# Kernel optimization log

Hardware: AMD Instinct MI355X
Metric: run time of the kernel (lower is better)

## Reference

```python
import jax, jax.numpy as jnp
import numpy as np

N, E, F_IN, HID, HEADS, NCLS = 50000, 800000, 512, 64, 4, 40
NEG_SLOPE = 0.2


def setup_inputs() -> dict:
    key = jax.random.key(0)
    ks = jax.random.split(key, 12)
    x = jax.random.normal(ks[0], (N, F_IN), jnp.float32)
    edge_index = jax.random.randint(ks[1], (2, E), 0, N, jnp.int32)
    edge_weight = jnp.ones((E,), jnp.float32)
    s1 = 1.0 / np.sqrt(F_IN)
    s2 = 1.0 / np.sqrt(HID * HEADS)
    return {
        "x": x,
        "edge_index": edge_index,
        "edge_weight": edge_weight,
        "W1": jax.random.normal(ks[2], (F_IN, HEADS * HID), jnp.float32) * s1,
        "a_src1": jax.random.normal(ks[3], (HEADS, HID), jnp.float32) * s1,
        "a_dst1": jax.random.normal(ks[4], (HEADS, HID), jnp.float32) * s1,
        "b1": jnp.zeros((HEADS * HID,), jnp.float32),
        "W2": jax.random.normal(ks[5], (HEADS * HID, NCLS), jnp.float32) * s2,
        "a_src2": jax.random.normal(ks[6], (1, NCLS), jnp.float32) * s2,
        "a_dst2": jax.random.normal(ks[7], (1, NCLS), jnp.float32) * s2,
        "b2": jnp.zeros((NCLS,), jnp.float32),
    }


def _gat_layer(x, src, dst, ew, W, a_s, a_d, b, heads, n):
    c = W.shape[1] // heads
    h = (x @ W).reshape(n, heads, c)                      # [N,H,C]
    alpha_s = jnp.einsum('nhc,hc->nh', h, a_s)            # [N,H]
    alpha_d = jnp.einsum('nhc,hc->nh', h, a_d)
    e = jax.nn.leaky_relu(alpha_s[src] + alpha_d[dst], NEG_SLOPE)  # [Et,H]
    # segment softmax over destination nodes (self-loops guarantee nonempty segs)
    m = jax.ops.segment_max(e, dst, num_segments=n)
    ex = jnp.exp(e - m[dst])
    denom = jax.ops.segment_sum(ex, dst, num_segments=n)
    alpha = ex / (denom[dst] + 1e-16)                     # [Et,H]
    alpha = alpha * ew[:, None]
    msg = h[src] * alpha[:, :, None]                      # [Et,H,C]
    out = jax.ops.segment_sum(msg, dst, num_segments=n)   # [N,H,C]
    return out.reshape(n, heads * c) + b


def reference(x, edge_index, edge_weight, W1, a_src1, a_dst1, b1, W2, a_src2, a_dst2, b2):
    n = x.shape[0]
    loop = jnp.arange(n, dtype=edge_index.dtype)
    src = jnp.concatenate([edge_index[0], loop])
    dst = jnp.concatenate([edge_index[1], loop])
    ew = jnp.concatenate([edge_weight, jnp.ones((n,), edge_weight.dtype)])
    h = _gat_layer(x, src, dst, ew, W1, a_src1, a_dst1, b1, HEADS, n)
    h = jax.nn.relu(h)  # dropout p=0.0, eval mode: no-op
    out = _gat_layer(h, src, dst, ew, W2, a_src2, a_dst2, b2, 1, n)
    return out  # Identity (log_softmax_return=False)
```

## Files before the change

kernel.cpp:

```cpp
#include <hip/hip_runtime.h>
#include <math.h>

#define N_NODES 50000
#define N_EDGES 800000
#define ET (N_EDGES + N_NODES)
#define F_IN 512
#define HID 64
#define HEADS 4
#define C1 (HEADS * HID)
#define NCLS 40
#define NEG_SLOPE 0.2f

#define BUK_SHIFT 7
#define BUK_NODES (1 << BUK_SHIFT)
#define NBUK ((N_NODES + BUK_NODES - 1) / BUK_NODES)
#define CAP 4096
#define NREP 4
#define SUBCAP (CAP / NREP)
#define BF_STRIDE 8
#define EPB_A 2048
#define NBLK_A ((ET + EPB_A - 1) / EPB_A)
#define NG1 ((N_NODES + 127) / 128)
#define RCAP 2560

typedef __attribute__((ext_vector_type(8))) short short8;
typedef __attribute__((ext_vector_type(4))) float floatx4;

__device__ __forceinline__ float leaky(float x) { return fmaxf(x, NEG_SLOPE * x); }

__device__ __forceinline__ unsigned short f2bf(float f) {
    unsigned u = __float_as_uint(f);
    u += 0x7fffu + ((u >> 16) & 1u);
    return (unsigned short)(u >> 16);
}
__device__ __forceinline__ float bf2f(unsigned short u) {
    return __uint_as_float(((unsigned)u) << 16);
}
__device__ __forceinline__ float bflo(unsigned v) { return __uint_as_float(v << 16); }
__device__ __forceinline__ float bfhi(unsigned v) { return __uint_as_float(v & 0xffff0000u); }

__device__ __forceinline__ void edge_sd(int e, const int* __restrict__ ei,
                                        const float* __restrict__ ew,
                                        int& s, int& d, float& w) {
    if (e < N_EDGES) { s = ei[e]; d = ei[N_EDGES + e]; w = ew[e]; }
    else             { s = d = e - N_EDGES; w = 1.f; }
}

__global__ void wt_prep_kernel(const float* __restrict__ W, unsigned short* __restrict__ WT,
                               int* __restrict__ bfill) {
    __shared__ float tile[32][33];
    int k0 = blockIdx.x * 32;
    int n0 = blockIdx.y * 32;
    int tx = threadIdx.x, ty = threadIdx.y;
    if (blockIdx.x == 0 && blockIdx.y == 0) {
        int tid = ty * 32 + tx;
        for (int i = tid; i < NBUK * NREP * BF_STRIDE; i += 256) bfill[i] = 0;
    }
    #pragma unroll
    for (int i = 0; i < 32; i += 8)
        tile[ty + i][tx] = W[(size_t)(k0 + ty + i) * C1 + n0 + tx];
    __syncthreads();
    #pragma unroll
    for (int i = 0; i < 32; i += 8)
        WT[(size_t)(n0 + ty + i) * F_IN + k0 + tx] = f2bf(tile[tx][ty + i]);
}

__global__ __launch_bounds__(512) void g1pa_kernel(const float* __restrict__ X,
                                                   const unsigned short* __restrict__ WT,
                                                   const float* __restrict__ a_s1,
                                                   const float* __restrict__ a_d1,
                                                   unsigned short* __restrict__ H,
                                                   float* __restrict__ AS,
                                                   float* __restrict__ AD,
                                                   const int* __restrict__ ei,
                                                   const float* __restrict__ ew,
                                                   int* __restrict__ bfill,
                                                   int2* __restrict__ SB) {
    __shared__ short As[128][40];
    __shared__ short Bs[256][40];
    __shared__ int lcnt[NBUK];
    __shared__ int lbase[NBUK];
    const int t = threadIdx.x;

    if (blockIdx.x >= NG1) {
        const int pb = blockIdx.x - NG1;
        const int rep = pb & (NREP - 1);
        const int e0 = pb * EPB_A + t;
        for (int i = t; i < NBUK; i += 512) lcnt[i] = 0;
        __syncthreads();
        int rx[4], ry[4];
        #pragma unroll
        for (int i = 0; i < 4; i++) {
            int e = e0 + i * 512;
            rx[i] = -1;
            ry[i] = 0;
            if (e < ET) {
                int s, d; float w;
                edge_sd(e, ei, ew, s, d, w);
                rx[i] = s | (d << 16);
                ry[i] = __float_as_int(w);
                atomicAdd(&lcnt[d >> BUK_SHIFT], 1);
            }
        }
        __syncthreads();
        for (int i = t; i < NBUK; i += 512) {
            int c = lcnt[i];
            lbase[i] = c ? atomicAdd(&bfill[(i * NREP + rep) * BF_STRIDE], c) : 0;
            lcnt[i] = 0;
        }
        __syncthreads();
        #pragma unroll
        for (int i = 0; i < 4; i++) {
            if (rx[i] != -1) {
                int b = ((unsigned)rx[i] >> 16) >> BUK_SHIFT;
                int r = atomicAdd(&lcnt[b], 1);
                int idx = lbase[b] + r;
                if (idx < SUBCAP)
                    SB[(size_t)b * CAP + rep * SUBCAP + idx] = make_int2(rx[i], ry[i]);
            }
        }
        return;
    }

    const int m0 = blockIdx.x * 128;
    const int lane = t & 63;
    const int wave = t >> 6;
    const int wm = wave >> 2;
    const int wn = wave & 3;
    const int l15 = lane & 15;
    const int quad = lane >> 4;

    const int ar = t >> 2;
    const int ac0 = (t & 3) * 8;
    const int gr = m0 + ar;
    const int bn = t >> 1;
    const int bc0 = (t & 1) * 16;

    floatx4 acc[4][4];
    #pragma unroll
    for (int i = 0; i < 4; i++)
        #pragma unroll
        for (int j = 0; j < 4; j++) acc[i][j] = (floatx4){0.f, 0.f, 0.f, 0.f};

    for (int k0 = 0; k0 < F_IN; k0 += 32) {
        float xv[8];
        if (gr < N_NODES) {
            const float4* p = (const float4*)(X + (size_t)gr * F_IN + k0 + ac0);
            float4 v0 = p[0], v1 = p[1];
            xv[0] = v0.x; xv[1] = v0.y; xv[2] = v0.z; xv[3] = v0.w;
            xv[4] = v1.x; xv[5] = v1.y; xv[6] = v1.z; xv[7] = v1.w;
        } else {
            #pragma unroll
            for (int i = 0; i < 8; i++) xv[i] = 0.f;
        }
        short8 av;
        #pragma unroll
        for (int i = 0; i < 8; i++) av[i] = (short)f2bf(xv[i]);
        *(short8*)&As[ar][ac0] = av;

        const short8* q = (const short8*)(WT + (size_t)bn * F_IN + k0 + bc0);
        *(short8*)&Bs[bn][bc0]     = q[0];
        *(short8*)&Bs[bn][bc0 + 8] = q[1];
        __syncthreads();

        short8 a[4], b[4];
        #pragma unroll
        for (int i = 0; i < 4; i++)
            a[i] = *(const short8*)&As[wm * 64 + i * 16 + l15][quad * 8];
        #pragma unroll
        for (int j = 0; j < 4; j++)
            b[j] = *(const short8*)&Bs[wn * 64 + j * 16 + l15][quad * 8];
        #pragma unroll
        for (int i = 0; i < 4; i++)
            #pragma unroll
            for (int j = 0; j < 4; j++)
                acc[i][j] = __builtin_amdgcn_mfma_f32_16x16x32_bf16(a[i], b[j], acc[i][j], 0, 0, 0);
        __syncthreads();
    }

    float asr[4], adr[4];
    #pragma unroll
    for (int j = 0; j < 4; j++) {
        asr[j] = a_s1[wn * HID + j * 16 + l15];
        adr[j] = a_d1[wn * HID + j * 16 + l15];
    }

    #pragma unroll
    for (int i = 0; i < 4; i++) {
        int rbase = m0 + wm * 64 + i * 16 + quad * 4;
        #pragma unroll
        for (int j = 0; j < 4; j++) {
            int col = wn * 64 + j * 16 + l15;
            #pragma unroll
            for (int r = 0; r < 4; r++) {
                int row = rbase + r;
                if (row < N_NODES) H[(size_t)row * C1 + col] = f2bf(acc[i][j][r]);
            }
        }
        #pragma unroll
        for (int r = 0; r < 4; r++) {
            int row = rbase + r;
            float s_ = acc[i][0][r] * asr[0] + acc[i][1][r] * asr[1]
                     + acc[i][2][r] * asr[2] + acc[i][3][r] * asr[3];
            float d_ = acc[i][0][r] * adr[0] + acc[i][1][r] * adr[1]
                     + acc[i][2][r] * adr[2] + acc[i][3][r] * adr[3];
            #pragma unroll
            for (int m = 8; m; m >>= 1) { s_ += __shfl_xor(s_, m); d_ += __shfl_xor(d_, m); }
            if (l15 == 0 && row < N_NODES) {
                AS[row * 4 + wn] = s_;
                AD[row * 4 + wn] = d_;
            }
        }
    }
}

__global__ __launch_bounds__(512) void place_kernel(const int* __restrict__ bfill,
                                                    const int2* __restrict__ SB,
                                                    int* __restrict__ row_ptr,
                                                    int2* __restrict__ E2) {
    __shared__ int2 rec[RCAP];
    __shared__ int lh[BUK_NODES];
    __shared__ int excl[BUK_NODES];
    __shared__ int psum[512];
    const int b = blockIdx.x;
    const int n0 = b << BUK_SHIFT;
    const int t = threadIdx.x;

    int v = 0;
    if (t < b) {
        #pragma unroll
        for (int r = 0; r < NREP; r++) {
            int c = bfill[(t * NREP + r) * BF_STRIDE];
            v += (c > SUBCAP) ? SUBCAP : c;
        }
    }
    psum[t] = v;
    __syncthreads();
    for (int s = 256; s > 0; s >>= 1) {
        if (t < s) psum[t] += psum[t + s];
        __syncthreads();
    }
    const int base_b = psum[0];

    int c[NREP], off[NREP];
    int tot = 0;
    #pragma unroll
    for (int r = 0; r < NREP; r++) {
        int cc = bfill[(b * NREP + r) * BF_STRIDE];
        c[r] = (cc > SUBCAP) ? SUBCAP : cc;
        off[r] = tot;
        tot += c[r];
    }
    if (t < BUK_NODES) lh[t] = 0;
    __syncthreads();
    #pragma unroll
    for (int r = 0; r < NREP; r++) {
        const int2* base = SB + (size_t)b * CAP + r * SUBCAP;
        for (int i = t; i < c[r]; i += 512) {
            int idx = off[r] + i;
            if (idx < RCAP) rec[idx] = base[i];
        }
    }
    if (tot > RCAP) tot = RCAP;
    __syncthreads();
    for (int i = t; i < tot; i += 512)
        atomicAdd(&lh[(((unsigned)rec[i].x) >> 16) - n0], 1);
    __syncthreads();
    if (t < BUK_NODES) excl[t] = lh[t];
    __syncthreads();
    #pragma unroll
    for (int s = 1; s < BUK_NODES; s <<= 1) {
        int u = (t < BUK_NODES && t >= s) ? excl[t - s] : 0;
        __syncthreads();
        if (t < BUK_NODES) excl[t] += u;
        __syncthreads();
    }
    if (t < BUK_NODES) {
        int e = excl[t] - lh[t];
        int node = n0 + t;
        if (node < N_NODES) row_ptr[node] = base_b + e;
        lh[t] = e;
    }
    __syncthreads();
    for (int i = t; i < tot; i += 512) {
        int2 v2 = rec[i];
        int d = (((unsigned)v2.x) >> 16) - n0;
        int pos = atomicAdd(&lh[d], 1);
        E2[base_b + pos] = make_int2(v2.x & 0xffff, v2.y);
    }
}

__global__ __launch_bounds__(256) void agg1_csr_kernel(const int* __restrict__ row_ptr,
                                                       const int2* __restrict__ E2,
                                                       const float* __restrict__ AS,
                                                       const float* __restrict__ AD,
                                                       const unsigned short* __restrict__ H,
                                                       const float* __restrict__ b1,
                                                       unsigned short* __restrict__ OUT) {
    int n = blockIdx.x * 4 + (threadIdx.x >> 6);
    int lane = threadIdx.x & 63;
    if (n >= N_NODES) return;
    int l15 = lane & 15;
    int h = lane >> 4;
    int c0 = lane * 4;
    int beg = row_ptr[n];
    int end = (n + 1 < N_NODES) ? row_ptr[n + 1] : ET;
    float ad = AD[n * 4 + h];
    float den = 0.f;
    float a0 = 0.f, a1 = 0.f, a2 = 0.f, a3 = 0.f;

    for (int base = beg; base < end; base += 16) {
        int m = end - base; if (m > 16) m = 16;
        float pw = 0.f; int s = 0;
        if (l15 < m) {
            int2 e = E2[base + l15];
            s = e.x;
            float pe = __expf(leaky(AS[e.x * 4 + h] + ad));
            den += pe;
            pw = pe * __int_as_float(e.y);
        }
        int p = 0;
        for (; p + 4 <= m; p += 4) {
            int s0 = __shfl(s, p);
            int s1 = __shfl(s, p + 1);
            int s2 = __shfl(s, p + 2);
            int s3 = __shfl(s, p + 3);
            uint2 u0 = *(const uint2*)(H + (size_t)s0 * C1 + c0);
            uint2 u1 = *(const uint2*)(H + (size_t)s1 * C1 + c0);
            uint2 u2 = *(const uint2*)(H + (size_t)s2 * C1 + c0);
            uint2 u3 = *(const uint2*)(H + (size_t)s3 * C1 + c0);
            float w0 = __shfl(pw, h * 16 + p);
            float w1 = __shfl(pw, h * 16 + p + 1);
            float w2 = __shfl(pw, h * 16 + p + 2);
            float w3 = __shfl(pw, h * 16 + p + 3);
            a0 += w0 * bflo(u0.x) + w1 * bflo(u1.x) + w2 * bflo(u2.x) + w3 * bflo(u3.x);
            a1 += w0 * bfhi(u0.x) + w1 * bfhi(u1.x) + w2 * bfhi(u2.x) + w3 * bfhi(u3.x);
            a2 += w0 * bflo(u0.y) + w1 * bflo(u1.y) + w2 * bflo(u2.y) + w3 * bflo(u3.y);
            a3 += w0 * bfhi(u0.y) + w1 * bfhi(u1.y) + w2 * bfhi(u2.y) + w3 * bfhi(u3.y);
        }
        for (; p < m; p++) {
            int s0 = __shfl(s, p);
            uint2 u0 = *(const uint2*)(H + (size_t)s0 * C1 + c0);
            float w0 = __shfl(pw, h * 16 + p);
            a0 += w0 * bflo(u0.x);
            a1 += w0 * bfhi(u0.x);
            a2 += w0 * bflo(u0.y);
            a3 += w0 * bfhi(u0.y);
        }
    }
    den += __shfl_xor(den, 1);
    den += __shfl_xor(den, 2);
    den += __shfl_xor(den, 4);
    den += __shfl_xor(den, 8);

    float r = 1.f / (den + 1e-16f);
    float4 bv = *(const float4*)(b1 + c0);
    float v0 = a0 * r + bv.x, v1 = a1 * r + bv.y, v2 = a2 * r + bv.z, v3 = a3 * r + bv.w;
    v0 = v0 > 0.f ? v0 : 0.f;
    v1 = v1 > 0.f ? v1 : 0.f;
    v2 = v2 > 0.f ? v2 : 0.f;
    v3 = v3 > 0.f ? v3 : 0.f;
    uint2 o;
    o.x = ((unsigned)f2bf(v1) << 16) | (unsigned)f2bf(v0);
    o.y = ((unsigned)f2bf(v3) << 16) | (unsigned)f2bf(v2);
    *(uint2*)(OUT + (size_t)n * C1 + c0) = o;
}

#define BROW 264
__global__ __launch_bounds__(512) void gemm2_mfma_kernel(const unsigned short* __restrict__ A,
                                                         const float* __restrict__ W2,
                                                         const float* __restrict__ a_s2,
                                                         const float* __restrict__ a_d2,
                                                         unsigned short* __restrict__ H2b,
                                                         float* __restrict__ AS2,
                                                         float* __restrict__ AD2) {
    __shared__ short As[256][40];
    __shared__ short Bs[48 * BROW];
    const int t = threadIdx.x;
    const int m0 = blockIdx.x * 256;
    const int lane = t & 63;
    const int wave = t >> 6;
    const int l15 = lane & 15;
    const int quad = lane >> 4;

    for (int i = t; i < 48 * 256; i += 512) {
        int n = i >> 8, k = i & 255;
        float v = (n < NCLS) ? W2[k * NCLS + n] : 0.f;
        Bs[n * BROW + k] = (short)f2bf(v);
    }

    const int ar = t >> 1;
    const int ac0 = (t & 1) * 16;

    floatx4 acc[2][3];
    #pragma unroll
    for (int i = 0; i < 2; i++)
        #pragma unroll
        for (int j = 0; j < 3; j++) acc[i][j] = (floatx4){0.f, 0.f, 0.f, 0.f};

    for (int k0 = 0; k0 < C1; k0 += 32) {
        const short8* q = (const short8*)(A + (size_t)(m0 + ar) * C1 + k0 + ac0);
        short8 v0 = q[0], v1 = q[1];
        __syncthreads();
        *(short8*)&As[ar][ac0]     = v0;
        *(short8*)&As[ar][ac0 + 8] = v1;
        __syncthreads();

        short8 a[2], b[3];
        #pragma unroll
        for (int i = 0; i < 2; i++)
            a[i] = *(const short8*)&As[wave * 32 + i * 16 + l15][quad * 8];
        #pragma unroll
        for (int j = 0; j < 3; j++)
            b[j] = *(const short8*)&Bs[(j * 16 + l15) * BROW + k0 + quad * 8];
        #pragma unroll
        for (int i = 0; i < 2; i++)
            #pragma unroll
            for (int j = 0; j < 3; j++)
                acc[i][j] = __builtin_amdgcn_mfma_f32_16x16x32_bf16(a[i], b[j], acc[i][j], 0, 0, 0);
    }

    float asr[3], adr[3];
    #pragma unroll
    for (int j = 0; j < 3; j++) {
        int col = j * 16 + l15;
        asr[j] = (col < NCLS) ? a_s2[col] : 0.f;
        adr[j] = (col < NCLS) ? a_d2[col] : 0.f;
    }

    #pragma unroll
    for (int i = 0; i < 2; i++) {
        #pragma unroll
        for (int r = 0; r < 4; r++) {
            int row = m0 + wave * 32 + i * 16 + quad * 4 + r;
            float s_ = acc[i][0][r] * asr[0] + acc[i][1][r] * asr[1] + acc[i][2][r] * asr[2];
            float d_ = acc[i][0][r] * adr[0] + acc[i][1][r] * adr[1] + acc[i][2][r] * adr[2];
            #pragma unroll
            for (int m = 8; m; m >>= 1) { s_ += __shfl_xor(s_, m); d_ += __shfl_xor(d_, m); }
            if (l15 == 0 && row < N_NODES) { AS2[row] = s_; AD2[row] = d_; }
            #pragma unroll
            for (int j = 0; j < 3; j++) {
                int col = j * 16 + l15;
                if (col < NCLS && row < N_NODES)
                    H2b[(size_t)row * NCLS + col] = f2bf(acc[i][j][r]);
            }
        }
    }
}

__global__ __launch_bounds__(256) void agg2_csr_kernel(const int* __restrict__ row_ptr,
                                                       const int2* __restrict__ E2,
                                                       const float* __restrict__ AS,
                                                       const float* __restrict__ AD,
                                                       const unsigned short* __restrict__ H2b,
                                                       const float* __restrict__ b2,
                                                       float* __restrict__ OUT) {
    int lane = threadIdx.x & 63;
    int n = blockIdx.x * 4 + (threadIdx.x >> 6);
    if (n >= N_NODES) return;
    int beg = row_ptr[n];
    int end = (n + 1 < N_NODES) ? row_ptr[n + 1] : ET;
    float ad = AD[n];
    bool act = lane < NCLS;
    float den = 0.f, acc = 0.f;

    for (int base = beg; base < end; base += 64) {
        int m = end - base; if (m > 64) m = 64;
        float pw = 0.f; int s = 0;
        if (lane < m) {
            int2 e = E2[base + lane];
            s = e.x;
            float pe = __expf(leaky(AS[e.x] + ad));
            den += pe;
            pw = pe * __int_as_float(e.y);
        }
        int p = 0;
        for (; p + 4 <= m; p += 4) {
            int s0 = __shfl(s, p);
            int s1 = __shfl(s, p + 1);
            int s2 = __shfl(s, p + 2);
            int s3 = __shfl(s, p + 3);
            float w0 = __shfl(pw, p);
            float w1 = __shfl(pw, p + 1);
            float w2 = __shfl(pw, p + 2);
            float w3 = __shfl(pw, p + 3);
            if (act) {
                float h0 = bf2f(H2b[(size_t)s0 * NCLS + lane]);
                float h1 = bf2f(H2b[(size_t)s1 * NCLS + lane]);
                float h2 = bf2f(H2b[(size_t)s2 * NCLS + lane]);
                float h3 = bf2f(H2b[(size_t)s3 * NCLS + lane]);
                acc += w0 * h0 + w1 * h1 + w2 * h2 + w3 * h3;
            }
        }
        for (; p < m; p++) {
            int s0 = __shfl(s, p);
            float w0 = __shfl(pw, p);
            if (act) acc += w0 * bf2f(H2b[(size_t)s0 * NCLS + lane]);
        }
    }
    den += __shfl_xor(den, 1);
    den += __shfl_xor(den, 2);
    den += __shfl_xor(den, 4);
    den += __shfl_xor(den, 8);
    den += __shfl_xor(den, 16);
    den += __shfl_xor(den, 32);
    if (act) {
        float r = 1.f / (den + 1e-16f);
        OUT[(size_t)n * NCLS + lane] = acc * r + b2[lane];
    }
}

extern "C" void kernel_launch(void* const* d_in, const int* in_sizes, int n_in,
                              void* d_out, int out_size, void* d_ws, size_t ws_size,
                              hipStream_t stream) {
    const float* x    = (const float*)d_in[0];
    const int*   ei   = (const int*)d_in[1];
    const float* ew   = (const float*)d_in[2];
    const float* W1   = (const float*)d_in[3];
    const float* a_s1 = (const float*)d_in[4];
    const float* a_d1 = (const float*)d_in[5];
    const float* b1   = (const float*)d_in[6];
    const float* W2   = (const float*)d_in[7];
    const float* a_s2 = (const float*)d_in[8];
    const float* a_d2 = (const float*)d_in[9];
    const float* b2   = (const float*)d_in[10];
    float* out = (float*)d_out;

    unsigned short* H1b  = (unsigned short*)d_ws;
    unsigned short* OUT1b = H1b + (size_t)N_NODES * C1;
    float* AS1  = (float*)(OUT1b + (size_t)N_NODES * C1);
    float* AD1  = AS1 + N_NODES * HEADS;
    int* row_ptr = (int*)(AD1 + N_NODES * HEADS);
    int* bfill = row_ptr + N_NODES;
    int2* E2  = (int2*)(bfill + NBUK * NREP * BF_STRIDE);
    unsigned short* WT = (unsigned short*)(E2 + ET);
    int2* SB = (int2*)(WT + (size_t)F_IN * C1);
    unsigned short* H2b = H1b;
    float* AS2  = (float*)(H2b + (size_t)N_NODES * NCLS);
    float* AD2  = AS2 + N_NODES;

    wt_prep_kernel<<<dim3(F_IN / 32, C1 / 32), dim3(32, 8), 0, stream>>>(W1, WT, bfill);

    g1pa_kernel<<<NG1 + NBLK_A, 512, 0, stream>>>(x, WT, a_s1, a_d1, H1b, AS1, AD1,
                                                  ei, ew, bfill, SB);

    place_kernel<<<NBUK, 512, 0, stream>>>(bfill, SB, row_ptr, E2);

    agg1_csr_kernel<<<(N_NODES + 3) / 4, 256, 0, stream>>>(row_ptr, E2, AS1, AD1, H1b, b1, OUT1b);

    gemm2_mfma_kernel<<<(N_NODES + 255) / 256, 512, 0, stream>>>(OUT1b, W2, a_s2, a_d2, H2b, AS2, AD2);
    agg2_csr_kernel<<<(N_NODES + 3) / 4, 256, 0, stream>>>(row_ptr, E2, AS2, AD2, H2b, b2, out);
}
```

Baseline: 317.4 us.

## Restructure gemm2 to smaller row tiles with whole-K A staging

The layer-2 GEMM now uses 64-row tiles with 256 threads, so 782 blocks are launched instead of 196 and the GPU's compute units are filled better. Each thread loads its full A row slice into registers up front, overlapping that load with the W2 conversion into shared memory, and then does a single sync. This removes the per-K-step double sync. It also adds a bounds guard on A rows. The trade-off is that each block re-converts the whole W2 into shared memory, so that setup work is repeated across four times as many blocks.

```diff
diff --git a/kernel.cpp b/kernel.cpp
--- a/kernel.cpp
+++ b/kernel.cpp
@@ -367,57 +367,57 @@
 }
 
 #define BROW 264
-__global__ __launch_bounds__(512) void gemm2_mfma_kernel(const unsigned short* __restrict__ A,
+__global__ __launch_bounds__(256) void gemm2_mfma_kernel(const unsigned short* __restrict__ A,
                                                          const float* __restrict__ W2,
                                                          const float* __restrict__ a_s2,
                                                          const float* __restrict__ a_d2,
                                                          unsigned short* __restrict__ H2b,
                                                          float* __restrict__ AS2,
                                                          float* __restrict__ AD2) {
-    __shared__ short As[256][40];
+    __shared__ short As[64][BROW];
     __shared__ short Bs[48 * BROW];
     const int t = threadIdx.x;
-    const int m0 = blockIdx.x * 256;
+    const int m0 = blockIdx.x * 64;
     const int lane = t & 63;
     const int wave = t >> 6;
     const int l15 = lane & 15;
     const int quad = lane >> 4;
 
-    for (int i = t; i < 48 * 256; i += 512) {
+    const int ar = t >> 2;
+    const int ac0 = (t & 3) * 64;
+    short8 av[8];
+    if (m0 + ar < N_NODES) {
+        const short8* q = (const short8*)(A + (size_t)(m0 + ar) * C1 + ac0);
+        #pragma unroll
+        for (int i = 0; i < 8; i++) av[i] = q[i];
+    } else {
+        #pragma unroll
+        for (int i = 0; i < 8; i++) av[i] = (short8){0,0,0,0,0,0,0,0};
+    }
+    for (int i = t; i < 48 * 256; i += 256) {
         int n = i >> 8, k = i & 255;
         float v = (n < NCLS) ? W2[k * NCLS + n] : 0.f;
         Bs[n * BROW + k] = (short)f2bf(v);
     }
-
-    const int ar = t >> 1;
-    const int ac0 = (t & 1) * 16;
-
-    floatx4 acc[2][3];
-    #pragma unroll
-    for (int i = 0; i < 2; i++)
-        #pragma unroll
-        for (int j = 0; j < 3; j++) acc[i][j] = (floatx4){0.f, 0.f, 0.f, 0.f};
-
+    #pragma unroll
+    for (int i = 0; i < 8; i++)
+        *(short8*)&As[ar][ac0 + i * 8] = av[i];
+    __syncthreads();
+
+    floatx4 acc[3];
+    #pragma unroll
+    for (int j = 0; j < 3; j++) acc[j] = (floatx4){0.f, 0.f, 0.f, 0.f};
+
+    #pragma unroll
     for (int k0 = 0; k0 < C1; k0 += 32) {
-        const short8* q = (const short8*)(A + (size_t)(m0 + ar) * C1 + k0 + ac0);
-        short8 v0 = q[0], v1 = q[1];
-        __syncthreads();
-        *(short8*)&As[ar][ac0]     = v0;
-        *(short8*)&As[ar][ac0 + 8] = v1;
-        __syncthreads();
-
-        short8 a[2], b[3];
-        #pragma unroll
-        for (int i = 0; i < 2; i++)
-            a[i] = *(const short8*)&As[wave * 32 + i * 16 + l15][quad * 8];
+        short8 a = *(const short8*)&As[wave * 16 + l15][k0 + quad * 8];
+        short8 b[3];
         #pragma unroll
         for (int j = 0; j < 3; j++)
             b[j] = *(const short8*)&Bs[(j * 16 + l15) * BROW + k0 + quad * 8];
         #pragma unroll
-        for (int i = 0; i < 2; i++)
-            #pragma unroll
-            for (int j = 0; j < 3; j++)
-                acc[i][j] = __builtin_amdgcn_mfma_f32_16x16x32_bf16(a[i], b[j], acc[i][j], 0, 0, 0);
+        for (int j = 0; j < 3; j++)
+            acc[j] = __builtin_amdgcn_mfma_f32_16x16x32_bf16(a, b[j], acc[j], 0, 0, 0);
     }
 
     float asr[3], adr[3];
@@ -429,21 +429,18 @@
     }
 
     #pragma unroll
-    for (int i = 0; i < 2; i++) {
-        #pragma unroll
-        for (int r = 0; r < 4; r++) {
-            int row = m0 + wave * 32 + i * 16 + quad * 4 + r;
-            float s_ = acc[i][0][r] * asr[0] + acc[i][1][r] * asr[1] + acc[i][2][r] * asr[2];
-            float d_ = acc[i][0][r] * adr[0] + acc[i][1][r] * adr[1] + acc[i][2][r] * adr[2];
-            #pragma unroll
-            for (int m = 8; m; m >>= 1) { s_ += __shfl_xor(s_, m); d_ += __shfl_xor(d_, m); }
-            if (l15 == 0 && row < N_NODES) { AS2[row] = s_; AD2[row] = d_; }
-            #pragma unroll
-            for (int j = 0; j < 3; j++) {
-                int col = j * 16 + l15;
-                if (col < NCLS && row < N_NODES)
-                    H2b[(size_t)row * NCLS + col] = f2bf(acc[i][j][r]);
-            }
+    for (int r = 0; r < 4; r++) {
+        int row = m0 + wave * 16 + quad * 4 + r;
+        float s_ = acc[0][r] * asr[0] + acc[1][r] * asr[1] + acc[2][r] * asr[2];
+        float d_ = acc[0][r] * adr[0] + acc[1][r] * adr[1] + acc[2][r] * adr[2];
+        #pragma unroll
+        for (int m = 8; m; m >>= 1) { s_ += __shfl_xor(s_, m); d_ += __shfl_xor(d_, m); }
+        if (l15 == 0 && row < N_NODES) { AS2[row] = s_; AD2[row] = d_; }
+        #pragma unroll
+        for (int j = 0; j < 3; j++) {
+            int col = j * 16 + l15;
+            if (col < NCLS && row < N_NODES)
+                H2b[(size_t)row * NCLS + col] = f2bf(acc[j][r]);
         }
     }
 }
@@ -548,6 +545,6 @@
 
     agg1_csr_kernel<<<(N_NODES + 3) / 4, 256, 0, stream>>>(row_ptr, E2, AS1, AD1, H1b, b1, OUT1b);
 
-    gemm2_mfma_kernel<<<(N_NODES + 255) / 256, 512, 0, stream>>>(OUT1b, W2, a_s2, a_d2, H2b, AS2, AD2);
+    gemm2_mfma_kernel<<<(N_NODES + 63) / 64, 256, 0, stream>>>(OUT1b, W2, a_s2, a_d2, H2b, AS2, AD2);
     agg2_csr_kernel<<<(N_NODES + 3) / 4, 256, 0, stream>>>(row_ptr, E2, AS2, AD2, H2b, b2, out);
 }
```

Measured after the change: 333.9 us. 5.2% more time.
